# Optimization experiments

Measured on AMD Instinct MI355X. Metric: run time of the kernel, lower is better.

## Reference

```python
import jax, jax.numpy as jnp
import numpy as np

N_FP = 235336   # n_fingerprint
N_WORD = 7844   # n_word
D = 10          # embed / hidden dim (hard-coded in module)
K = 23          # conv kernel 2*11+1
PAD = 11
N_ATOMS = 4096
L_WORDS = 65536


def setup_inputs() -> dict:
    key = jax.random.key(0)
    ks = jax.random.split(key, 16)
    s = 0.1  # weight init scale
    return {
        "fingerprints": jax.random.randint(ks[0], (N_ATOMS,), 0, N_FP),
        # scale adjacency so x + A@hs stays O(1) over 3 layers
        "adjacency": jax.random.uniform(ks[1], (N_ATOMS, N_ATOMS), dtype=jnp.float32) * (1.0 / N_ATOMS),
        "words": jax.random.randint(ks[2], (L_WORDS,), 0, N_WORD),
        "embed_fp": jax.random.normal(ks[3], (N_FP, D), dtype=jnp.float32) * s,
        "embed_word": jax.random.normal(ks[4], (N_WORD, D), dtype=jnp.float32) * s,
        "W_gnn_w": jax.random.normal(ks[5], (3, D, D), dtype=jnp.float32) * s,
        "W_gnn_b": jax.random.normal(ks[6], (3, D), dtype=jnp.float32) * s,
        "W_cnn_w": jax.random.normal(ks[7], (3, 1, 1, K, K), dtype=jnp.float32) * (s / K),
        "W_cnn_b": jax.random.normal(ks[8], (3,), dtype=jnp.float32) * s,
        "W_att_w": jax.random.normal(ks[9], (D, D), dtype=jnp.float32) * s,
        "W_att_b": jax.random.normal(ks[10], (D,), dtype=jnp.float32) * s,
        "W_out_w": jax.random.normal(ks[11], (3, 2 * D, 2 * D), dtype=jnp.float32) * s,
        "W_out_b": jax.random.normal(ks[12], (3, 2 * D), dtype=jnp.float32) * s,
        "W_int_w": jax.random.normal(ks[13], (2, 2 * D), dtype=jnp.float32) * s,
        "W_int_b": jax.random.normal(ks[14], (2,), dtype=jnp.float32) * s,
    }


def reference(fingerprints, adjacency, words, embed_fp, embed_word,
              W_gnn_w, W_gnn_b, W_cnn_w, W_cnn_b, W_att_w, W_att_b,
              W_out_w, W_out_b, W_int_w, W_int_b):
    # ---- Compound vector with GNN ----
    xs = embed_fp[fingerprints]                       # [N, D]
    for i in range(3):                                # fixed 3 layers
        hs = jax.nn.relu(xs @ W_gnn_w[i].T + W_gnn_b[i])
        xs = xs + adjacency @ hs                      # dense message passing
    compound = jnp.mean(xs, axis=0, keepdims=True)    # [1, D]

    # ---- Protein vector with attention-CNN ----
    ws = embed_word[words]                            # [L, D]
    t = ws[None, None]                                # [1,1,L,D] NCHW
    for i in range(3):
        t = jax.nn.relu(
            jax.lax.conv_general_dilated(t, W_cnn_w[i], (1, 1),
                                          [(PAD, PAD), (PAD, PAD)])
            + W_cnn_b[i])
    xs_p = t[0, 0]                                    # [L, D]

    h = jax.nn.relu(compound @ W_att_w.T + W_att_b)   # [1, D]
    hs_p = jax.nn.relu(xs_p @ W_att_w.T + W_att_b)    # [L, D]
    weights = jnp.tanh(h @ hs_p.T)                    # [1, L]
    ys = weights.T * hs_p                             # [L, D]
    protein = jnp.mean(ys, axis=0, keepdims=True)     # [1, D]

    # ---- Fusion MLP ----
    cat = jnp.concatenate([compound, protein], axis=1)  # [1, 2D]
    for j in range(3):
        cat = jax.nn.relu(cat @ W_out_w[j].T + W_out_b[j])
    return cat @ W_int_w.T + W_int_b                  # [1, 2]
```

## Files before the change

kernel.cpp:

```cpp
#include <hip/hip_runtime.h>
#include <hip/hip_bf16.h>
#include <math.h>

#define N_ATOMS 4096
#define L_WORDS 65536
#define DD 10
#define HALO 11

__global__ __launch_bounds__(256) void gnn_embed(
    const int* __restrict__ fp, const float* __restrict__ embed_fp,
    const float* __restrict__ Wg0, const float* __restrict__ bg0,
    float* __restrict__ xs0, float* __restrict__ hsT0)
{
    int n = blockIdx.x * blockDim.x + threadIdx.x;
    if (n >= N_ATOMS) return;
    float x[DD];
    const float* e = embed_fp + (size_t)fp[n] * DD;
    #pragma unroll
    for (int d = 0; d < DD; ++d) { x[d] = e[d]; xs0[n * DD + d] = x[d]; }
    #pragma unroll
    for (int d = 0; d < DD; ++d) {
        float v = bg0[d];
        #pragma unroll
        for (int k = 0; k < DD; ++k) v += Wg0[d * DD + k] * x[k];
        hsT0[d * N_ATOMS + n] = fmaxf(v, 0.f);
    }
}

#define GP_BLOCK 256
#define GP_RPW 4
#define GP_ROWS_BLK 16
#define GP_QCOLS 1024
#define CONV_BLOCKS 256
#define CONV_BLOCK 256

__global__ __launch_bounds__(256, 4) void fused_layer(
    const float* __restrict__ A,
    const float* __restrict__ hsT_in,
    float* __restrict__ part,
    const float* __restrict__ tin,
    const int* __restrict__ words,
    const float* __restrict__ embed_word,
    const float* __restrict__ w,
    const float* __restrict__ bptr,
    float* __restrict__ tout)
{
    __shared__ float sh[DD * GP_QCOLS];
    const int tid = threadIdx.x;

    if (blockIdx.x < CONV_BLOCKS) {
        float* s = sh;
        const int l0 = blockIdx.x * CONV_BLOCK;

        for (int idx = tid; idx < (CONV_BLOCK + 2 * HALO) * DD; idx += CONV_BLOCK) {
            int rr = idx / DD, d = idx - rr * DD;
            int gr = l0 - HALO + rr;
            float v = 0.f;
            if (gr >= 0 && gr < L_WORDS) {
                if (tin) v = tin[(size_t)gr * DD + d];
                else     v = embed_word[(size_t)words[gr] * DD + d];
            }
            s[rr * 11 + d] = v;
        }
        __syncthreads();

        const float bias = *bptr;
        float acc[DD];
        #pragma unroll
        for (int d = 0; d < DD; ++d) acc[d] = bias;

        for (int i = 0; i < 23; ++i) {
            float row[DD];
            const float* sr = &s[(tid + i) * 11];
            #pragma unroll
            for (int c = 0; c < DD; ++c) row[c] = sr[c];
            #pragma unroll
            for (int d = 0; d < DD; ++d) {
                #pragma unroll
                for (int c = 0; c < DD; ++c)
                    acc[d] += row[c] * w[i * 23 + (c - d + 11)];
            }
        }
        const int l = l0 + tid;
        #pragma unroll
        for (int d = 0; d < DD; ++d)
            tout[(size_t)l * DD + d] = fmaxf(acc[d], 0.f);
    } else {
        const int b = blockIdx.x - CONV_BLOCKS;
        const int wave = tid >> 6, lane = tid & 63;
        const int q = b & 3, rg = b >> 2;
        const int qbase = q * GP_QCOLS;

        {
            const float4* src = (const float4*)(hsT_in + qbase);
            float4* dst = (float4*)sh;
            #pragma unroll
            for (int k = 0; k < DD; ++k)
                dst[k * 256 + tid] = src[k * (N_ATOMS / 4) + tid];
        }
        __syncthreads();

        const int r0 = rg * GP_ROWS_BLK + wave * GP_RPW;
        const float4* Ar[GP_RPW];
        #pragma unroll
        for (int r = 0; r < GP_RPW; ++r)
            Ar[r] = (const float4*)(A + (size_t)(r0 + r) * N_ATOMS + qbase);
        const float4* sh4 = (const float4*)sh;

        float acc[GP_RPW][DD];
        #pragma unroll
        for (int r = 0; r < GP_RPW; ++r)
            #pragma unroll
            for (int d = 0; d < DD; ++d) acc[r][d] = 0.f;

        #pragma unroll
        for (int it = 0; it < GP_QCOLS / 256; ++it) {
            const int cb = it * 64 + lane;
            float4 a[GP_RPW];
            #pragma unroll
            for (int r = 0; r < GP_RPW; ++r) a[r] = Ar[r][cb];
            #pragma unroll
            for (int d = 0; d < DD; ++d) {
                float4 h = sh4[d * 256 + cb];
                #pragma unroll
                for (int r = 0; r < GP_RPW; ++r) {
                    acc[r][d] += a[r].x * h.x;
                    acc[r][d] += a[r].y * h.y;
                    acc[r][d] += a[r].z * h.z;
                    acc[r][d] += a[r].w * h.w;
                }
            }
        }

        #pragma unroll
        for (int m = 32; m >= 1; m >>= 1) {
            #pragma unroll
            for (int r = 0; r < GP_RPW; ++r)
                #pragma unroll
                for (int d = 0; d < DD; ++d)
                    acc[r][d] += __shfl_xor(acc[r][d], m, 64);
        }

        if (lane == 0) {
            #pragma unroll
            for (int r = 0; r < GP_RPW; ++r)
                #pragma unroll
                for (int d = 0; d < DD; ++d)
                    part[((size_t)q * N_ATOMS + r0 + r) * DD + d] = acc[r][d];
        }
    }
}

__global__ __launch_bounds__(256) void gnn_combine(
    const float* __restrict__ xs_in,
    const float* __restrict__ part,
    float* __restrict__ xs_out,
    float* __restrict__ hsT_out,
    const float* __restrict__ Wg,
    const float* __restrict__ bg,
    float* __restrict__ comp_part)
{
    const int tid = threadIdx.x, wave = tid >> 6, lane = tid & 63;
    const int n = blockIdx.x * 256 + tid;

    float x[DD];
    #pragma unroll
    for (int d = 0; d < DD; ++d) {
        float v = xs_in[n * DD + d];
        #pragma unroll
        for (int q = 0; q < 4; ++q)
            v += part[((size_t)q * N_ATOMS + n) * DD + d];
        x[d] = v;
        xs_out[n * DD + d] = v;
    }
    if (hsT_out) {
        #pragma unroll
        for (int d = 0; d < DD; ++d) {
            float v = bg[d];
            #pragma unroll
            for (int k = 0; k < DD; ++k) v += Wg[d * DD + k] * x[k];
            hsT_out[(size_t)d * N_ATOMS + n] = fmaxf(v, 0.f);
        }
    }
    if (comp_part) {
        #pragma unroll
        for (int m = 32; m >= 1; m >>= 1) {
            #pragma unroll
            for (int d = 0; d < DD; ++d) x[d] += __shfl_xor(x[d], m, 64);
        }
        __shared__ float s[4][DD];
        if (lane == 0) {
            #pragma unroll
            for (int d = 0; d < DD; ++d) s[wave][d] = x[d];
        }
        __syncthreads();
        if (tid < DD)
            comp_part[blockIdx.x * DD + tid] =
                s[0][tid] + s[1][tid] + s[2][tid] + s[3][tid];
    }
}

__global__ __launch_bounds__(256) void reduce_comp(
    const float* __restrict__ part, int npart, float* __restrict__ comp)
{
    const int tid = threadIdx.x, wave = tid >> 6, lane = tid & 63;
    float v[DD];
    #pragma unroll
    for (int d = 0; d < DD; ++d) v[d] = 0.f;
    for (int p = tid; p < npart; p += 256) {
        #pragma unroll
        for (int d = 0; d < DD; ++d) v[d] += part[p * DD + d];
    }
    #pragma unroll
    for (int off = 32; off >= 1; off >>= 1) {
        #pragma unroll
        for (int d = 0; d < DD; ++d) v[d] += __shfl_down(v[d], off, 64);
    }
    __shared__ float s[4][DD];
    if (lane == 0) {
        #pragma unroll
        for (int d = 0; d < DD; ++d) s[wave][d] = v[d];
    }
    __syncthreads();
    if (tid < DD)
        comp[tid] = (s[0][tid] + s[1][tid] + s[2][tid] + s[3][tid]) * (1.f / N_ATOMS);
}

__global__ __launch_bounds__(1024) void attention_pool(
    const float* __restrict__ xs_p,
    const float* __restrict__ comp,
    const float* __restrict__ Wa, const float* __restrict__ ba,
    float* __restrict__ att_part)
{
    const int tid = threadIdx.x, wave = tid >> 6, lane = tid & 63;
    const int l = blockIdx.x * 1024 + tid;

    float h[DD];
    #pragma unroll
    for (int d = 0; d < DD; ++d) {
        float v = ba[d];
        #pragma unroll
        for (int k = 0; k < DD; ++k) v += Wa[d * DD + k] * comp[k];
        h[d] = fmaxf(v, 0.f);
    }

    float row[DD];
    #pragma unroll
    for (int d = 0; d < DD; ++d) row[d] = xs_p[(size_t)l * DD + d];

    float hp[DD], dotv = 0.f;
    #pragma unroll
    for (int d = 0; d < DD; ++d) {
        float v = ba[d];
        #pragma unroll
        for (int k = 0; k < DD; ++k) v += Wa[d * DD + k] * row[k];
        hp[d] = fmaxf(v, 0.f);
        dotv += h[d] * hp[d];
    }
    const float wgt = tanhf(dotv);

    float y[DD];
    #pragma unroll
    for (int d = 0; d < DD; ++d) y[d] = wgt * hp[d];

    #pragma unroll
    for (int off = 32; off >= 1; off >>= 1) {
        #pragma unroll
        for (int d = 0; d < DD; ++d) y[d] += __shfl_down(y[d], off, 64);
    }
    __shared__ float s[16][DD];
    if (lane == 0) {
        #pragma unroll
        for (int d = 0; d < DD; ++d) s[wave][d] = y[d];
    }
    __syncthreads();
    if (tid < DD) {
        float v = 0.f;
        #pragma unroll
        for (int wv = 0; wv < 16; ++wv) v += s[wv][tid];
        att_part[blockIdx.x * DD + tid] = v;
    }
}

__global__ __launch_bounds__(64) void final_mlp(
    const float* __restrict__ comp,
    const float* __restrict__ att_part,
    const float* __restrict__ Wo, const float* __restrict__ bo,
    const float* __restrict__ Wi, const float* __restrict__ bi,
    float* __restrict__ out)
{
    const int t = threadIdx.x;
    float a[DD];
    #pragma unroll
    for (int d = 0; d < DD; ++d) a[d] = att_part[t * DD + d];
    #pragma unroll
    for (int off = 32; off >= 1; off >>= 1) {
        #pragma unroll
        for (int d = 0; d < DD; ++d) a[d] += __shfl_down(a[d], off, 64);
    }

    __shared__ float cat[20];
    if (t < DD) cat[t] = comp[t];
    if (t == 0) {
        #pragma unroll
        for (int d = 0; d < DD; ++d) cat[DD + d] = a[d] * (1.f / L_WORDS);
    }
    __syncthreads();

    for (int j = 0; j < 3; ++j) {
        float v = 0.f;
        if (t < 20) {
            v = bo[j * 20 + t];
            for (int k = 0; k < 20; ++k) v += Wo[j * 400 + t * 20 + k] * cat[k];
        }
        __syncthreads();
        if (t < 20) cat[t] = fmaxf(v, 0.f);
        __syncthreads();
    }
    if (t < 2) {
        float v = bi[t];
        for (int k = 0; k < 20; ++k) v += Wi[t * 20 + k] * cat[k];
        out[t] = v;
    }
}

extern "C" void kernel_launch(void* const* d_in, const int* in_sizes, int n_in,
                              void* d_out, int out_size, void* d_ws, size_t ws_size,
                              hipStream_t stream)
{
    const int*   fp     = (const int*)d_in[0];
    const float* A      = (const float*)d_in[1];
    const int*   words  = (const int*)d_in[2];
    const float* emb_fp = (const float*)d_in[3];
    const float* emb_w  = (const float*)d_in[4];
    const float* Wg     = (const float*)d_in[5];
    const float* bg     = (const float*)d_in[6];
    const float* Wc     = (const float*)d_in[7];
    const float* bc     = (const float*)d_in[8];
    const float* Wa     = (const float*)d_in[9];
    const float* ba     = (const float*)d_in[10];
    const float* Wo     = (const float*)d_in[11];
    const float* bo     = (const float*)d_in[12];
    const float* Wi     = (const float*)d_in[13];
    const float* bi     = (const float*)d_in[14];
    float* out = (float*)d_out;
    float* ws  = (float*)d_ws;

    float* xs0  = ws;
    float* xs1  = ws + 40960;
    float* hsT0 = ws + 81920;
    float* hsT1 = ws + 122880;
    float* t0   = ws + 163840;
    float* t1   = ws + 163840 + 655360;
    float* comp = ws + 163840 + 2 * 655360;
    float* part = comp + 16;
    float* comp_part = part + 163840;
    float* att_part  = comp_part + 256;

    const int fused_grid = CONV_BLOCKS + (N_ATOMS / GP_ROWS_BLK) * 4;

    gnn_embed<<<N_ATOMS / 256, 256, 0, stream>>>(fp, emb_fp, Wg, bg, xs0, hsT0);

    fused_layer<<<fused_grid, 256, 0, stream>>>(
        A, hsT0, part, nullptr, words, emb_w, Wc, bc, t0);
    gnn_combine<<<N_ATOMS / 256, 256, 0, stream>>>(
        xs0, part, xs1, hsT1, Wg + 100, bg + 10, nullptr);

    fused_layer<<<fused_grid, 256, 0, stream>>>(
        A, hsT1, part, t0, nullptr, nullptr, Wc + 529, bc + 1, t1);
    gnn_combine<<<N_ATOMS / 256, 256, 0, stream>>>(
        xs1, part, xs0, hsT0, Wg + 200, bg + 20, nullptr);

    fused_layer<<<fused_grid, 256, 0, stream>>>(
        A, hsT0, part, t1, nullptr, nullptr, Wc + 1058, bc + 2, t0);
    gnn_combine<<<N_ATOMS / 256, 256, 0, stream>>>(
        xs0, part, xs1, nullptr, nullptr, nullptr, comp_part);
    reduce_comp<<<1, 256, 0, stream>>>(comp_part, 16, comp);

    attention_pool<<<L_WORDS / 1024, 1024, 0, stream>>>(t0, comp, Wa, ba, att_part);
    final_mlp<<<1, 64, 0, stream>>>(comp, att_part, Wo, bo, Wi, bi, out);
}
```

Before: 233.6 us.

## Fuse GNN combine into layer kernel, recompute hs from partials, enlarge row tiles

Removes the separate gnn_combine and reduce_comp kernels. Each GNN block now rebuilds x from xs0 plus the earlier layers' partial sums and computes relu(Wx+b) into shared memory itself. The matvec tile grows to 8 rows per wave and 32 rows per block, with launch bounds lowered to 2. The compound mean reduction is folded into attention_pool and final_mlp, trimming launches and intermediate writes at the cost of redundant per-block recomputation of hs and more register pressure.

```diff
diff --git a/kernel.cpp b/kernel.cpp
--- a/kernel.cpp
+++ b/kernel.cpp
@@ -7,51 +7,41 @@
 #define DD 10
 #define HALO 11
 
+#define CONV_BLOCKS 256
+#define CONV_BLOCK 256
+#define GNN_BLOCKS 512
+#define RPW 8
+#define RPB 32
+#define QCOLS 1024
+
 __global__ __launch_bounds__(256) void gnn_embed(
     const int* __restrict__ fp, const float* __restrict__ embed_fp,
-    const float* __restrict__ Wg0, const float* __restrict__ bg0,
-    float* __restrict__ xs0, float* __restrict__ hsT0)
+    float* __restrict__ xs0)
 {
     int n = blockIdx.x * blockDim.x + threadIdx.x;
     if (n >= N_ATOMS) return;
-    float x[DD];
     const float* e = embed_fp + (size_t)fp[n] * DD;
     #pragma unroll
-    for (int d = 0; d < DD; ++d) { x[d] = e[d]; xs0[n * DD + d] = x[d]; }
-    #pragma unroll
-    for (int d = 0; d < DD; ++d) {
-        float v = bg0[d];
-        #pragma unroll
-        for (int k = 0; k < DD; ++k) v += Wg0[d * DD + k] * x[k];
-        hsT0[d * N_ATOMS + n] = fmaxf(v, 0.f);
-    }
-}
-
-#define GP_BLOCK 256
-#define GP_RPW 4
-#define GP_ROWS_BLK 16
-#define GP_QCOLS 1024
-#define CONV_BLOCKS 256
-#define CONV_BLOCK 256
-
-__global__ __launch_bounds__(256, 4) void fused_layer(
+    for (int d = 0; d < DD; ++d) xs0[n * DD + d] = e[d];
+}
+
+__global__ __launch_bounds__(256, 2) void fused_layer(
     const float* __restrict__ A,
-    const float* __restrict__ hsT_in,
+    const float* __restrict__ xs0,
+    const float* __restrict__ p0,
+    const float* __restrict__ p1,
     float* __restrict__ part,
-    const float* __restrict__ tin,
-    const int* __restrict__ words,
-    const float* __restrict__ embed_word,
-    const float* __restrict__ w,
-    const float* __restrict__ bptr,
-    float* __restrict__ tout)
-{
-    __shared__ float sh[DD * GP_QCOLS];
+    const float* __restrict__ Wg, const float* __restrict__ bg,
+    const float* __restrict__ tin, const int* __restrict__ words,
+    const float* __restrict__ embed_word, const float* __restrict__ w,
+    const float* __restrict__ bptr, float* __restrict__ tout)
+{
+    __shared__ float sh[DD * QCOLS];
     const int tid = threadIdx.x;
 
     if (blockIdx.x < CONV_BLOCKS) {
         float* s = sh;
         const int l0 = blockIdx.x * CONV_BLOCK;
-
         for (int idx = tid; idx < (CONV_BLOCK + 2 * HALO) * DD; idx += CONV_BLOCK) {
             int rr = idx / DD, d = idx - rr * DD;
             int gr = l0 - HALO + rr;
@@ -68,7 +58,6 @@
         float acc[DD];
         #pragma unroll
         for (int d = 0; d < DD; ++d) acc[d] = bias;
-
         for (int i = 0; i < 23; ++i) {
             float row[DD];
             const float* sr = &s[(tid + i) * 11];
@@ -89,41 +78,59 @@
         const int b = blockIdx.x - CONV_BLOCKS;
         const int wave = tid >> 6, lane = tid & 63;
         const int q = b & 3, rg = b >> 2;
-        const int qbase = q * GP_QCOLS;
-
-        {
-            const float4* src = (const float4*)(hsT_in + qbase);
-            float4* dst = (float4*)sh;
-            #pragma unroll
-            for (int k = 0; k < DD; ++k)
-                dst[k * 256 + tid] = src[k * (N_ATOMS / 4) + tid];
+        const int qbase = q * QCOLS;
+
+        for (int j = 0; j < 4; ++j) {
+            const int lc = j * 256 + tid;
+            const int n = qbase + lc;
+            float x[DD];
+            #pragma unroll
+            for (int d = 0; d < DD; ++d) x[d] = xs0[n * DD + d];
+            if (p0) {
+                #pragma unroll
+                for (int qq = 0; qq < 4; ++qq)
+                    #pragma unroll
+                    for (int d = 0; d < DD; ++d)
+                        x[d] += p0[((size_t)qq * N_ATOMS + n) * DD + d];
+            }
+            if (p1) {
+                #pragma unroll
+                for (int qq = 0; qq < 4; ++qq)
+                    #pragma unroll
+                    for (int d = 0; d < DD; ++d)
+                        x[d] += p1[((size_t)qq * N_ATOMS + n) * DD + d];
+            }
+            #pragma unroll
+            for (int d = 0; d < DD; ++d) {
+                float v = bg[d];
+                #pragma unroll
+                for (int k = 0; k < DD; ++k) v += Wg[d * DD + k] * x[k];
+                sh[d * QCOLS + lc] = fmaxf(v, 0.f);
+            }
         }
         __syncthreads();
 
-        const int r0 = rg * GP_ROWS_BLK + wave * GP_RPW;
-        const float4* Ar[GP_RPW];
-        #pragma unroll
-        for (int r = 0; r < GP_RPW; ++r)
-            Ar[r] = (const float4*)(A + (size_t)(r0 + r) * N_ATOMS + qbase);
+        const int r0 = rg * RPB + wave * RPW;
+        const float4* A4 = (const float4*)(A + (size_t)r0 * N_ATOMS) + q * (QCOLS / 4);
         const float4* sh4 = (const float4*)sh;
 
-        float acc[GP_RPW][DD];
-        #pragma unroll
-        for (int r = 0; r < GP_RPW; ++r)
+        float acc[RPW][DD];
+        #pragma unroll
+        for (int r = 0; r < RPW; ++r)
             #pragma unroll
             for (int d = 0; d < DD; ++d) acc[r][d] = 0.f;
 
-        #pragma unroll
-        for (int it = 0; it < GP_QCOLS / 256; ++it) {
+        #pragma unroll 2
+        for (int it = 0; it < 4; ++it) {
             const int cb = it * 64 + lane;
-            float4 a[GP_RPW];
-            #pragma unroll
-            for (int r = 0; r < GP_RPW; ++r) a[r] = Ar[r][cb];
+            float4 a[RPW];
+            #pragma unroll
+            for (int r = 0; r < RPW; ++r) a[r] = A4[r * (N_ATOMS / 4) + cb];
             #pragma unroll
             for (int d = 0; d < DD; ++d) {
                 float4 h = sh4[d * 256 + cb];
                 #pragma unroll
-                for (int r = 0; r < GP_RPW; ++r) {
+                for (int r = 0; r < RPW; ++r) {
                     acc[r][d] += a[r].x * h.x;
                     acc[r][d] += a[r].y * h.y;
                     acc[r][d] += a[r].z * h.z;
@@ -135,15 +142,14 @@
         #pragma unroll
         for (int m = 32; m >= 1; m >>= 1) {
             #pragma unroll
-            for (int r = 0; r < GP_RPW; ++r)
+            for (int r = 0; r < RPW; ++r)
                 #pragma unroll
                 for (int d = 0; d < DD; ++d)
                     acc[r][d] += __shfl_xor(acc[r][d], m, 64);
         }
-
         if (lane == 0) {
             #pragma unroll
-            for (int r = 0; r < GP_RPW; ++r)
+            for (int r = 0; r < RPW; ++r)
                 #pragma unroll
                 for (int d = 0; d < DD; ++d)
                     part[((size_t)q * N_ATOMS + r0 + r) * DD + d] = acc[r][d];
@@ -151,96 +157,65 @@
     }
 }
 
-__global__ __launch_bounds__(256) void gnn_combine(
-    const float* __restrict__ xs_in,
-    const float* __restrict__ part,
-    float* __restrict__ xs_out,
-    float* __restrict__ hsT_out,
-    const float* __restrict__ Wg,
-    const float* __restrict__ bg,
+__global__ __launch_bounds__(256) void comp_reduce(
+    const float* __restrict__ xs0, const float* __restrict__ p0,
+    const float* __restrict__ p1, const float* __restrict__ p2,
     float* __restrict__ comp_part)
 {
     const int tid = threadIdx.x, wave = tid >> 6, lane = tid & 63;
     const int n = blockIdx.x * 256 + tid;
-
     float x[DD];
     #pragma unroll
     for (int d = 0; d < DD; ++d) {
-        float v = xs_in[n * DD + d];
-        #pragma unroll
-        for (int q = 0; q < 4; ++q)
-            v += part[((size_t)q * N_ATOMS + n) * DD + d];
+        float v = xs0[n * DD + d];
+        #pragma unroll
+        for (int qq = 0; qq < 4; ++qq) {
+            v += p0[((size_t)qq * N_ATOMS + n) * DD + d];
+            v += p1[((size_t)qq * N_ATOMS + n) * DD + d];
+            v += p2[((size_t)qq * N_ATOMS + n) * DD + d];
+        }
         x[d] = v;
-        xs_out[n * DD + d] = v;
-    }
-    if (hsT_out) {
-        #pragma unroll
-        for (int d = 0; d < DD; ++d) {
-            float v = bg[d];
-            #pragma unroll
-            for (int k = 0; k < DD; ++k) v += Wg[d * DD + k] * x[k];
-            hsT_out[(size_t)d * N_ATOMS + n] = fmaxf(v, 0.f);
-        }
-    }
-    if (comp_part) {
-        #pragma unroll
-        for (int m = 32; m >= 1; m >>= 1) {
-            #pragma unroll
-            for (int d = 0; d < DD; ++d) x[d] += __shfl_xor(x[d], m, 64);
-        }
-        __shared__ float s[4][DD];
-        if (lane == 0) {
-            #pragma unroll
-            for (int d = 0; d < DD; ++d) s[wave][d] = x[d];
-        }
-        __syncthreads();
-        if (tid < DD)
-            comp_part[blockIdx.x * DD + tid] =
-                s[0][tid] + s[1][tid] + s[2][tid] + s[3][tid];
-    }
-}
-
-__global__ __launch_bounds__(256) void reduce_comp(
-    const float* __restrict__ part, int npart, float* __restrict__ comp)
-{
-    const int tid = threadIdx.x, wave = tid >> 6, lane = tid & 63;
-    float v[DD];
-    #pragma unroll
-    for (int d = 0; d < DD; ++d) v[d] = 0.f;
-    for (int p = tid; p < npart; p += 256) {
-        #pragma unroll
-        for (int d = 0; d < DD; ++d) v[d] += part[p * DD + d];
-    }
-    #pragma unroll
-    for (int off = 32; off >= 1; off >>= 1) {
-        #pragma unroll
-        for (int d = 0; d < DD; ++d) v[d] += __shfl_down(v[d], off, 64);
+    }
+    #pragma unroll
+    for (int m = 32; m >= 1; m >>= 1) {
+        #pragma unroll
+        for (int d = 0; d < DD; ++d) x[d] += __shfl_xor(x[d], m, 64);
     }
     __shared__ float s[4][DD];
     if (lane == 0) {
         #pragma unroll
-        for (int d = 0; d < DD; ++d) s[wave][d] = v[d];
+        for (int d = 0; d < DD; ++d) s[wave][d] = x[d];
     }
     __syncthreads();
     if (tid < DD)
-        comp[tid] = (s[0][tid] + s[1][tid] + s[2][tid] + s[3][tid]) * (1.f / N_ATOMS);
+        comp_part[blockIdx.x * DD + tid] =
+            s[0][tid] + s[1][tid] + s[2][tid] + s[3][tid];
 }
 
 __global__ __launch_bounds__(1024) void attention_pool(
-    const float* __restrict__ xs_p,
-    const float* __restrict__ comp,
+    const float* __restrict__ xs_p, const float* __restrict__ comp_part,
     const float* __restrict__ Wa, const float* __restrict__ ba,
     float* __restrict__ att_part)
 {
+    __shared__ float shc[DD];
+    __shared__ float s[16][DD];
     const int tid = threadIdx.x, wave = tid >> 6, lane = tid & 63;
     const int l = blockIdx.x * 1024 + tid;
 
+    if (tid < DD) {
+        float c = 0.f;
+        #pragma unroll
+        for (int p = 0; p < 16; ++p) c += comp_part[p * DD + tid];
+        shc[tid] = c * (1.f / N_ATOMS);
+    }
+    __syncthreads();
+
     float h[DD];
     #pragma unroll
     for (int d = 0; d < DD; ++d) {
         float v = ba[d];
         #pragma unroll
-        for (int k = 0; k < DD; ++k) v += Wa[d * DD + k] * comp[k];
+        for (int k = 0; k < DD; ++k) v += Wa[d * DD + k] * shc[k];
         h[d] = fmaxf(v, 0.f);
     }
 
@@ -262,13 +237,11 @@
     float y[DD];
     #pragma unroll
     for (int d = 0; d < DD; ++d) y[d] = wgt * hp[d];
-
-    #pragma unroll
-    for (int off = 32; off >= 1; off >>= 1) {
-        #pragma unroll
-        for (int d = 0; d < DD; ++d) y[d] += __shfl_down(y[d], off, 64);
-    }
-    __shared__ float s[16][DD];
+    #pragma unroll
+    for (int m = 32; m >= 1; m >>= 1) {
+        #pragma unroll
+        for (int d = 0; d < DD; ++d) y[d] += __shfl_xor(y[d], m, 64);
+    }
     if (lane == 0) {
         #pragma unroll
         for (int d = 0; d < DD; ++d) s[wave][d] = y[d];
@@ -283,8 +256,7 @@
 }
 
 __global__ __launch_bounds__(64) void final_mlp(
-    const float* __restrict__ comp,
-    const float* __restrict__ att_part,
+    const float* __restrict__ comp_part, const float* __restrict__ att_part,
     const float* __restrict__ Wo, const float* __restrict__ bo,
     const float* __restrict__ Wi, const float* __restrict__ bi,
     float* __restrict__ out)
@@ -294,19 +266,22 @@
     #pragma unroll
     for (int d = 0; d < DD; ++d) a[d] = att_part[t * DD + d];
     #pragma unroll
-    for (int off = 32; off >= 1; off >>= 1) {
-        #pragma unroll
-        for (int d = 0; d < DD; ++d) a[d] += __shfl_down(a[d], off, 64);
-    }
-
+    for (int m = 32; m >= 1; m >>= 1) {
+        #pragma unroll
+        for (int d = 0; d < DD; ++d) a[d] += __shfl_xor(a[d], m, 64);
+    }
     __shared__ float cat[20];
-    if (t < DD) cat[t] = comp[t];
+    if (t < DD) {
+        float c = 0.f;
+        #pragma unroll
+        for (int p = 0; p < 16; ++p) c += comp_part[p * DD + t];
+        cat[t] = c * (1.f / N_ATOMS);
+    }
     if (t == 0) {
         #pragma unroll
         for (int d = 0; d < DD; ++d) cat[DD + d] = a[d] * (1.f / L_WORDS);
     }
     __syncthreads();
-
     for (int j = 0; j < 3; ++j) {
         float v = 0.f;
         if (t < 20) {
@@ -346,37 +321,35 @@
     float* out = (float*)d_out;
     float* ws  = (float*)d_ws;
 
-    float* xs0  = ws;
-    float* xs1  = ws + 40960;
-    float* hsT0 = ws + 81920;
-    float* hsT1 = ws + 122880;
-    float* t0   = ws + 163840;
-    float* t1   = ws + 163840 + 655360;
-    float* comp = ws + 163840 + 2 * 655360;
-    float* part = comp + 16;
-    float* comp_part = part + 163840;
-    float* att_part  = comp_part + 256;
-
-    const int fused_grid = CONV_BLOCKS + (N_ATOMS / GP_ROWS_BLK) * 4;
-
-    gnn_embed<<<N_ATOMS / 256, 256, 0, stream>>>(fp, emb_fp, Wg, bg, xs0, hsT0);
+    float* xs0   = ws;
+    float* ta    = ws + 40960;
+    float* tb    = ws + 696320;
+    float* part0 = ws + 1351680;
+    float* part1 = ws + 1515520;
+    float* part2 = ws + 1679360;
+    float* comp_part = ws + 1843200;
+    float* att_part  = ws + 1843456;
+
+    const int fused_grid = CONV_BLOCKS + GNN_BLOCKS;
+
+    gnn_embed<<<N_ATOMS / 256, 256, 0, stream>>>(fp, emb_fp, xs0);
 
     fused_layer<<<fused_grid, 256, 0, stream>>>(
-        A, hsT0, part, nullptr, words, emb_w, Wc, bc, t0);
-    gnn_combine<<<N_ATOMS / 256, 256, 0, stream>>>(
-        xs0, part, xs1, hsT1, Wg + 100, bg + 10, nullptr);
+        A, xs0, nullptr, nullptr, part0, Wg, bg,
+        nullptr, words, emb_w, Wc, bc, ta);
 
     fused_layer<<<fused_grid, 256, 0, stream>>>(
-        A, hsT1, part, t0, nullptr, nullptr, Wc + 529, bc + 1, t1);
-    gnn_combine<<<N_ATOMS / 256, 256, 0, stream>>>(
-        xs1, part, xs0, hsT0, Wg + 200, bg + 20, nullptr);
+        A, xs0, part0, nullptr, part1, Wg + 100, bg + 10,
+        ta, nullptr, nullptr, Wc + 529, bc + 1, tb);
 
     fused_layer<<<fused_grid, 256, 0, stream>>>(
-        A, hsT0, part, t1, nullptr, nullptr, Wc + 1058, bc + 2, t0);
-    gnn_combine<<<N_ATOMS / 256, 256, 0, stream>>>(
-        xs0, part, xs1, nullptr, nullptr, nullptr, comp_part);
-    reduce_comp<<<1, 256, 0, stream>>>(comp_part, 16, comp);
-
-    attention_pool<<<L_WORDS / 1024, 1024, 0, stream>>>(t0, comp, Wa, ba, att_part);
-    final_mlp<<<1, 64, 0, stream>>>(comp, att_part, Wo, bo, Wi, bi, out);
-}
+        A, xs0, part0, part1, part2, Wg + 200, bg + 20,
+        tb, nullptr, nullptr, Wc + 1058, bc + 2, ta);
+
+    comp_reduce<<<16, 256, 0, stream>>>(xs0, part0, part1, part2, comp_part);
+
+    attention_pool<<<L_WORDS / 1024, 1024, 0, stream>>>(
+        ta, comp_part, Wa, ba, att_part);
+
+    final_mlp<<<1, 64, 0, stream>>>(comp_part, att_part, Wo, bo, Wi, bi, out);
+}
```

Result: faster. 210.8 us (-9.7%).
